# Optimization experiments

Hardware: AMD Instinct MI355X
Metric: run time of the kernel (lower is better)

The kernel has to match this reference:

```python
import jax, jax.numpy as jnp
import numpy as np

N_NODES = 20000
N_EDGES = 320000
N_GRAPHS = 64
IN_DIM = 768
HID = 256
HEADS = 4
NUM_CLASSES = 5
NEG_SLOPE = 0.2  # PyG GATConv default leaky_relu slope


def setup_inputs() -> dict:
    key = jax.random.key(0)
    ks = jax.random.split(key, 20)
    x = jax.random.normal(ks[0], (N_NODES, IN_DIM), dtype=jnp.float32)
    edge_index = jax.random.randint(ks[1], (2, N_EDGES), 0, N_NODES, dtype=jnp.int32)
    batch = jnp.sort(jax.random.randint(ks[2], (N_NODES,), 0, N_GRAPHS, dtype=jnp.int32))
    s = lambda k, sh: jax.random.normal(k, sh, dtype=jnp.float32) * (1.0 / np.sqrt(sh[0]))
    HC = HEADS * HID
    return {
        "x": x, "edge_index": edge_index, "batch": batch,
        "Wp": s(ks[3], (IN_DIM, HID)), "bp": jnp.zeros((HID,), jnp.float32),
        "W1": s(ks[4], (HID, HC)),
        "as1": jax.random.normal(ks[5], (HEADS, HID)) * 0.1,
        "ad1": jax.random.normal(ks[6], (HEADS, HID)) * 0.1,
        "b1": jnp.zeros((HC,), jnp.float32),
        "W2": s(ks[7], (HC, HC)),
        "as2": jax.random.normal(ks[8], (HEADS, HID)) * 0.1,
        "ad2": jax.random.normal(ks[9], (HEADS, HID)) * 0.1,
        "b2": jnp.zeros((HC,), jnp.float32),
        "Wc1": s(ks[10], (2 * HC, 256)), "bc1": jnp.zeros((256,), jnp.float32),
        "Wc2": s(ks[11], (256, NUM_CLASSES)), "bc2": jnp.zeros((NUM_CLASSES,), jnp.float32),
    }


def _gat(h, src, dst, W, att_s, att_d, bias):
    # PyG GATConv (concat=True), dropout in eval mode (identity).
    N = h.shape[0]
    hW = (h @ W).reshape(N, HEADS, HID)             # [N,H,C]
    a_s = jnp.einsum('nhc,hc->nh', hW, att_s)        # per-node src score
    a_d = jnp.einsum('nhc,hc->nh', hW, att_d)
    e = jax.nn.leaky_relu(a_s[src] + a_d[dst], NEG_SLOPE)  # [E,H]
    # segment softmax over incoming edges of each destination node
    m = jax.ops.segment_max(e, dst, num_segments=N)
    e = jnp.exp(e - m[dst])
    denom = jax.ops.segment_sum(e, dst, num_segments=N)
    alpha = e / (denom[dst] + 1e-16)
    msg = hW[src] * alpha[:, :, None]                # [E,H,C]
    out = jax.ops.segment_sum(msg, dst, num_segments=N)
    return out.reshape(N, HEADS * HID) + bias


def reference(x, edge_index, batch, Wp, bp, W1, as1, ad1, b1, W2, as2, ad2, b2, Wc1, bc1, Wc2, bc2):
    N = x.shape[0]
    # add self-loops (PyG GATConv default add_self_loops=True)
    loop = jnp.arange(N, dtype=edge_index.dtype)
    src = jnp.concatenate([edge_index[0], loop])
    dst = jnp.concatenate([edge_index[1], loop])

    h = jax.nn.relu(x @ Wp + bp)
    h = jax.nn.elu(_gat(h, src, dst, W1, as1, ad1, b1))
    h = jax.nn.elu(_gat(h, src, dst, W2, as2, ad2, b2))

    # global mean / max pool over graphs
    cnt = jax.ops.segment_sum(jnp.ones((N,), h.dtype), batch, num_segments=N_GRAPHS)
    mean_pool = jax.ops.segment_sum(h, batch, num_segments=N_GRAPHS) / jnp.maximum(cnt, 1.0)[:, None]
    max_pool = jax.ops.segment_max(h, batch, num_segments=N_GRAPHS)
    g = jnp.concatenate([mean_pool, max_pool], axis=1)  # [G, 2*H*C]

    hcls = jax.nn.relu(g @ Wc1 + bc1)
    return hcls @ Wc2 + bc2
```

## Files before the change

kernel.cpp:

```cpp
#include <hip/hip_runtime.h>
#include <hip/hip_fp16.h>
#include <math.h>

#define N_HID 256
#define N_HEADS 4
#define N_HC 1024
#define N_GRAPHS 64

typedef __attribute__((ext_vector_type(4))) float f32x4;
typedef _Float16 half8 __attribute__((ext_vector_type(8)));
typedef _Float16 half4 __attribute__((ext_vector_type(4)));

__device__ __forceinline__ void gl_lds16h(const __half* g, __half* l) {
    __builtin_amdgcn_global_load_lds(
        (const __attribute__((address_space(1))) unsigned int*)g,
        (__attribute__((address_space(3))) unsigned int*)l, 16, 0, 0);
}

__global__ __launch_bounds__(256) void k_deg(const int* __restrict__ dst, int E,
                                             int* __restrict__ deg) {
    int e = blockIdx.x * 256 + threadIdx.x;
    if (e < E) atomicAdd(&deg[dst[e]], 1);
}

__global__ __launch_bounds__(1024) void k_scan(const int* __restrict__ deg,
                                               int* __restrict__ rowstart, int N) {
    __shared__ int part[1024];
    const int t = threadIdx.x;
    const int chunk = (N + 1023) / 1024;
    const int c0 = t * chunk;
    int s = 0;
    for (int i = 0; i < chunk; i++) {
        int idx = c0 + i;
        if (idx < N) s += deg[idx];
    }
    part[t] = s;
    __syncthreads();
    for (int off = 1; off < 1024; off <<= 1) {
        int v = (t >= off) ? part[t - off] : 0;
        __syncthreads();
        part[t] += v;
        __syncthreads();
    }
    int run = (t == 0) ? 0 : part[t - 1];
    if (t == 0) rowstart[0] = 0;
    for (int i = 0; i < chunk; i++) {
        int idx = c0 + i;
        if (idx < N) {
            run += deg[idx];
            rowstart[idx + 1] = run;
        }
    }
}

__global__ __launch_bounds__(256) void k_fill(const int* __restrict__ src,
                                              const int* __restrict__ dst, int E,
                                              const int* __restrict__ rowstart,
                                              int* __restrict__ cursor,
                                              int* __restrict__ col) {
    int e = blockIdx.x * 256 + threadIdx.x;
    if (e < E) {
        int d = dst[e];
        int p = atomicAdd(&cursor[d], 1);
        col[rowstart[d] + p] = src[e];
    }
}

__global__ __launch_bounds__(256) void k_wtt(const float* __restrict__ W,
                                             __half* __restrict__ WT, int K, int N) {
    __shared__ float tile[32][33];
    const int k0 = blockIdx.y * 32, n0 = blockIdx.x * 32;
    const int tr = threadIdx.x >> 5, tc = threadIdx.x & 31;
#pragma unroll
    for (int rr = 0; rr < 4; rr++) {
        int k = k0 + tr + rr * 8;
        tile[tr + rr * 8][tc] = W[(size_t)k * N + n0 + tc];
    }
    __syncthreads();
#pragma unroll
    for (int rr = 0; rr < 4; rr++) {
        int n = n0 + tr + rr * 8;
        WT[(size_t)n * K + k0 + tc] = __float2half(tile[tc][tr + rr * 8]);
    }
}

__global__ __launch_bounds__(256) void k_makeva(const __half* __restrict__ W1T,
                                                const float* __restrict__ as1,
                                                const float* __restrict__ ad1,
                                                float* __restrict__ va) {
    __shared__ float satt[256];
    int b = blockIdx.x;
    int h = b & 3, isd = b >> 2;
    int k = threadIdx.x;
    const float* att = (isd ? ad1 : as1) + h * 256;
    satt[k] = att[k];
    __syncthreads();
    const __half* wr = W1T + (size_t)(h * 256) * 256 + k;
    float s = 0.f;
    for (int c = 0; c < 256; c++) s += __half2float(wr[(size_t)c * 256]) * satt[c];
    va[b * 256 + k] = s;
}

__global__ __launch_bounds__(256) void k_makeva2(const __half* __restrict__ W2T,
                                                 const float* __restrict__ as2,
                                                 const float* __restrict__ ad2,
                                                 float* __restrict__ va2) {
    __shared__ float satt[256];
    int b = blockIdx.x;
    int h = b & 3;
    int t = threadIdx.x;
    const float* att = (b >= 4 ? ad2 : as2) + h * 256;
    satt[t] = att[t];
    __syncthreads();
    float s0 = 0.f, s1 = 0.f, s2 = 0.f, s3 = 0.f;
    const __half* base = W2T + (size_t)(h * 256) * 1024 + t * 4;
    for (int j = 0; j < 256; j++) {
        half4 wv = *reinterpret_cast<const half4*>(base + (size_t)j * 1024);
        float a = satt[j];
        s0 += a * (float)wv[0]; s1 += a * (float)wv[1];
        s2 += a * (float)wv[2]; s3 += a * (float)wv[3];
    }
    *(float4*)&va2[b * 1024 + t * 4] = make_float4(s0, s1, s2, s3);
}

template <int EPI, int COSCHED>
__global__ __launch_bounds__(256) void k_gemm2p(
    const __half* __restrict__ A, const __half* __restrict__ BT,
    const float* __restrict__ bias, __half* __restrict__ C,
    int M, int NROW, int K, int lda, int ldc,
    int aoffz, int boffz, int coffz, int bofz) {
    __shared__ __half sA[2][128 * 32];
    __shared__ __half sB[2][128 * 32];
    int bm, bn;
    size_t coff = 0;
    if (COSCHED) {
        const int bid = blockIdx.x;
        const int xcd = bid & 7, j0 = bid >> 3;
        const int br = xcd + 8 * (j0 >> 3);
        const int bc = j0 & 7;
        if (br >= NROW) return;
        bm = br * 128; bn = bc * 128;
    } else {
        const int z = blockIdx.z;
        A += (size_t)z * aoffz;
        BT += (size_t)z * boffz;
        bias += z * bofz;
        coff = (size_t)z * coffz;
        bm = blockIdx.y * 128; bn = blockIdx.x * 128;
    }
    const int tid = threadIdx.x, lane = tid & 63, w = tid >> 6;
    const int wr = (w >> 1) * 64, wc = (w & 1) * 64;
    const bool isB = (w >= 2);
    const __half* gsrc = isB ? (BT + (size_t)bn * K) : (A + (size_t)bm * lda);
    const int gld = isB ? K : lda;
    const int rbase = (w & 1) * 64;
    const int lr = lane >> 2, lsl = lane & 3;
    const int g = lane >> 4, fr = lane & 15;
    const int nt = K >> 5;

    f32x4 acc[4][4] = {};

    auto STAGE = [&](int b, int t) {
        __half* sbuf = (isB ? sB[b] : sA[b]);
        const int k0 = t << 5;
#pragma unroll
        for (int c2 = 0; c2 < 4; c2++) {
            int row = rbase + c2 * 16 + lr;
            int slg = lsl ^ ((row >> 1) & 3);
            gl_lds16h(gsrc + (size_t)row * gld + k0 + slg * 8,
                      sbuf + (rbase + c2 * 16) * 32);
        }
    };

    STAGE(0, 0);
    __syncthreads();
    int cur = 0;
    for (int t = 0; t < nt; ++t) {
        if (t + 1 < nt) STAGE(cur ^ 1, t + 1);
        half8 af[4], bf[4];
#pragma unroll
        for (int i = 0; i < 4; i++) {
            int Ra = wr + i * 16 + fr;
            af[i] = *reinterpret_cast<const half8*>(
                &sA[cur][Ra * 32 + ((g ^ ((Ra >> 1) & 3)) << 3)]);
            int Rb = wc + i * 16 + fr;
            bf[i] = *reinterpret_cast<const half8*>(
                &sB[cur][Rb * 32 + ((g ^ ((Rb >> 1) & 3)) << 3)]);
        }
#pragma unroll
        for (int i = 0; i < 4; i++)
#pragma unroll
            for (int j = 0; j < 4; j++)
                acc[i][j] = __builtin_amdgcn_mfma_f32_16x16x32_f16(af[i], bf[j], acc[i][j], 0, 0, 0);
        __syncthreads();
        cur ^= 1;
    }
    const int crow0 = (lane >> 4) * 4, ccol = lane & 15;
#pragma unroll
    for (int i = 0; i < 4; i++)
#pragma unroll
        for (int j = 0; j < 4; j++) {
            int cc = bn + wc + j * 16 + ccol;
            float bv = (EPI == 2) ? bias[cc] : 0.f;
#pragma unroll
            for (int r = 0; r < 4; r++) {
                int row = bm + wr + i * 16 + crow0 + r;
                if (row < M) {
                    float v = acc[i][j][r];
                    if (EPI == 2) { v += bv; v = v > 0.f ? v : (__expf(v) - 1.f); }
                    C[(size_t)row * ldc + coff + cc] = __float2half(v);
                }
            }
        }
}

__global__ __launch_bounds__(256) void k_gemm_x(
    const float* __restrict__ A, const __half* __restrict__ BT,
    const float* __restrict__ bias, __half* __restrict__ C,
    int M, int NROW, int K, int lda) {
    __shared__ __half sA[128 * 32];
    __shared__ __half sB[128 * 32];
    const int bid = blockIdx.x;
    const int xcd = bid & 7, j0 = bid >> 3;
    const int br = xcd + 8 * (j0 >> 1);
    const int bc = j0 & 1;
    if (br >= NROW) return;
    const int bm = br * 128, bn = bc * 128;
    const int tid = threadIdx.x, lane = tid & 63, w = tid >> 6;
    const int wr = (w >> 1) * 64, wc = (w & 1) * 64;
    const int sm = tid >> 1, skb = (tid & 1) * 16;
    const bool rok = (bm + sm) < M;
    const int ph0 = (((tid & 1) * 2 + 0) ^ ((sm >> 1) & 3)) << 3;
    const int ph1 = (((tid & 1) * 2 + 1) ^ ((sm >> 1) & 3)) << 3;
    const int lr = lane >> 2, lsl = lane & 3;

    f32x4 acc[4][4] = {};

    for (int k0 = 0; k0 < K; k0 += 32) {
#pragma unroll
        for (int c = 0; c < 2; c++) {
            int rb = (w + c * 4) * 16;
            int row = rb + lr;
            int slg = lsl ^ ((row >> 1) & 3);
            gl_lds16h(BT + (size_t)(bn + row) * K + k0 + slg * 8, sB + rb * 32);
        }
        {
            const float* Arow = A + (size_t)(bm + sm) * lda + k0 + skb;
            float4 v0 = make_float4(0.f, 0.f, 0.f, 0.f), v1 = v0, v2 = v0, v3 = v0;
            if (rok) {
                v0 = *(const float4*)(Arow + 0);
                v1 = *(const float4*)(Arow + 4);
                v2 = *(const float4*)(Arow + 8);
                v3 = *(const float4*)(Arow + 12);
            }
            half8 ha, hb;
            ha[0] = (_Float16)v0.x; ha[1] = (_Float16)v0.y;
            ha[2] = (_Float16)v0.z; ha[3] = (_Float16)v0.w;
            ha[4] = (_Float16)v1.x; ha[5] = (_Float16)v1.y;
            ha[6] = (_Float16)v1.z; ha[7] = (_Float16)v1.w;
            hb[0] = (_Float16)v2.x; hb[1] = (_Float16)v2.y;
            hb[2] = (_Float16)v2.z; hb[3] = (_Float16)v2.w;
            hb[4] = (_Float16)v3.x; hb[5] = (_Float16)v3.y;
            hb[6] = (_Float16)v3.z; hb[7] = (_Float16)v3.w;
            *reinterpret_cast<half8*>(&sA[sm * 32 + ph0]) = ha;
            *reinterpret_cast<half8*>(&sA[sm * 32 + ph1]) = hb;
        }
        __syncthreads();
        half8 af[4], bf[4];
        const int g = lane >> 4, fr = lane & 15;
#pragma unroll
        for (int i = 0; i < 4; i++) {
            int Ra = wr + i * 16 + fr;
            af[i] = *reinterpret_cast<const half8*>(
                &sA[Ra * 32 + ((g ^ ((Ra >> 1) & 3)) << 3)]);
            int Rb = wc + i * 16 + fr;
            bf[i] = *reinterpret_cast<const half8*>(
                &sB[Rb * 32 + ((g ^ ((Rb >> 1) & 3)) << 3)]);
        }
#pragma unroll
        for (int i = 0; i < 4; i++)
#pragma unroll
            for (int j = 0; j < 4; j++)
                acc[i][j] = __builtin_amdgcn_mfma_f32_16x16x32_f16(af[i], bf[j], acc[i][j], 0, 0, 0);
        __syncthreads();
    }
    const int crow0 = (lane >> 4) * 4, ccol = lane & 15;
#pragma unroll
    for (int i = 0; i < 4; i++)
#pragma unroll
        for (int j = 0; j < 4; j++) {
            int cc = bn + wc + j * 16 + ccol;
            float bv = bias[cc];
#pragma unroll
            for (int r = 0; r < 4; r++) {
                int row = bm + wr + i * 16 + crow0 + r;
                if (row < M) {
                    float v = acc[i][j][r] + bv;
                    v = v > 0.f ? v : 0.f;
                    C[(size_t)row * 256 + cc] = __float2half(v);
                }
            }
        }
}

__global__ __launch_bounds__(256) void k_score8(const __half* __restrict__ h0,
                                                const float* __restrict__ va,
                                                float* __restrict__ a_s,
                                                float* __restrict__ a_d, int N) {
    __shared__ float sva[8][256];
    int t = threadIdx.x;
    for (int i = t; i < 2048; i += 256) sva[i >> 8][i & 255] = va[i];
    __syncthreads();
    int wv = t >> 6, lane = t & 63;
    int n = blockIdx.x * 4 + wv;
    if (n >= N) return;
    uint2 u = *(const uint2*)(h0 + (size_t)n * 256 + lane * 4);
    __half2 q0 = __builtin_bit_cast(__half2, u.x);
    __half2 q1 = __builtin_bit_cast(__half2, u.y);
    float v0 = __half2float(q0.x), v1 = __half2float(q0.y);
    float v2 = __half2float(q1.x), v3 = __half2float(q1.y);
    float p[8];
#pragma unroll
    for (int v = 0; v < 8; v++) {
        p[v] = v0 * sva[v][lane * 4] + v1 * sva[v][lane * 4 + 1] +
               v2 * sva[v][lane * 4 + 2] + v3 * sva[v][lane * 4 + 3];
    }
#pragma unroll
    for (int off = 32; off > 0; off >>= 1)
#pragma unroll
        for (int v = 0; v < 8; v++) p[v] += __shfl_xor(p[v], off, 64);
    if (lane == 0) {
        *(float4*)&a_s[n * 4] = make_float4(p[0], p[1], p[2], p[3]);
        *(float4*)&a_d[n * 4] = make_float4(p[4], p[5], p[6], p[7]);
    }
}

__global__ __launch_bounds__(256) void k_score1024(const __half* __restrict__ h1,
                                                   const float* __restrict__ va2,
                                                   float* __restrict__ a_s,
                                                   float* __restrict__ a_d, int N) {
    __shared__ float sva[8 * 1024];
    int t = threadIdx.x;
    for (int i = t; i < 8192; i += 256) sva[i] = va2[i];
    __syncthreads();
    int wv = t >> 6, lane = t & 63;
    int n = blockIdx.x * 4 + wv;
    if (n >= N) return;
    const __half* hp = h1 + (size_t)n * 1024;
    float hv[16];
#pragma unroll
    for (int seg = 0; seg < 4; seg++) {
        half4 u = *reinterpret_cast<const half4*>(hp + seg * 256 + lane * 4);
#pragma unroll
        for (int c = 0; c < 4; c++) hv[seg * 4 + c] = (float)u[c];
    }
    float p[8] = {};
#pragma unroll
    for (int v = 0; v < 8; v++) {
#pragma unroll
        for (int seg = 0; seg < 4; seg++) {
            float4 f = *(const float4*)&sva[v * 1024 + seg * 256 + lane * 4];
            p[v] += hv[seg * 4] * f.x + hv[seg * 4 + 1] * f.y +
                    hv[seg * 4 + 2] * f.z + hv[seg * 4 + 3] * f.w;
        }
    }
#pragma unroll
    for (int off = 32; off > 0; off >>= 1)
#pragma unroll
        for (int v = 0; v < 8; v++) p[v] += __shfl_xor(p[v], off, 64);
    if (lane == 0) {
        *(float4*)&a_s[n * 4] = make_float4(p[0], p[1], p[2], p[3]);
        *(float4*)&a_d[n * 4] = make_float4(p[4], p[5], p[6], p[7]);
    }
}

__global__ __launch_bounds__(256) void k_gat_w1(
    const __half* __restrict__ h0, const float* __restrict__ a_s,
    const float* __restrict__ a_d, const int* __restrict__ rowstart,
    const int* __restrict__ col, __half* __restrict__ agg1, int N) {
    __shared__ int wsn[4][64];
    __shared__ float wal[4][64][2];
    const int w = threadIdx.x >> 6, lane = threadIdx.x & 63;
    const int ni = w >> 1, q = w & 1;
    const int n = blockIdx.x * 2 + ni;
    if (n >= N) return;
    const int hh0 = q * 2;
    const int e0 = rowstart[n];
    const int deg = rowstart[n + 1] - e0;
    const int tot = deg + 1;
    const float adv0 = a_d[n * 4 + hh0], adv1 = a_d[n * 4 + hh0 + 1];
    float M0 = -INFINITY, M1 = -INFINITY, S0 = 0.f, S1 = 0.f;
    float acc0[4] = {}, acc1[4] = {};

    for (int base = 0; base < tot; base += 64) {
        const int cnt = min(64, tot - base);
        const bool act = lane < cnt;
        int sn = n;
        float ev0 = -INFINITY, ev1 = -INFINITY;
        if (act) {
            const int li = base + lane;
            sn = (li < deg) ? col[e0 + li] : n;
            float s0 = a_s[sn * 4 + hh0] + adv0;
            float s1 = a_s[sn * 4 + hh0 + 1] + adv1;
            ev0 = s0 >= 0.f ? s0 : 0.2f * s0;
            ev1 = s1 >= 0.f ? s1 : 0.2f * s1;
        }
        float m0 = ev0, m1 = ev1;
#pragma unroll
        for (int off = 32; off > 0; off >>= 1) {
            m0 = fmaxf(m0, __shfl_xor(m0, off, 64));
            m1 = fmaxf(m1, __shfl_xor(m1, off, 64));
        }
        m0 = fmaxf(m0, M0); m1 = fmaxf(m1, M1);
        float w0 = act ? __expf(ev0 - m0) : 0.f;
        float w1 = act ? __expf(ev1 - m1) : 0.f;
        wsn[w][lane] = sn;
        wal[w][lane][0] = w0;
        wal[w][lane][1] = w1;
        float s0 = w0, s1 = w1;
#pragma unroll
        for (int off = 32; off > 0; off >>= 1) {
            s0 += __shfl_xor(s0, off, 64);
            s1 += __shfl_xor(s1, off, 64);
        }
        float sc0 = __expf(M0 - m0), sc1 = __expf(M1 - m1);
        S0 = S0 * sc0 + s0; S1 = S1 * sc1 + s1;
        M0 = m0; M1 = m1;
#pragma unroll
        for (int c = 0; c < 4; c++) { acc0[c] *= sc0; acc1[c] *= sc1; }
#pragma unroll 2
        for (int i = 0; i < cnt; i++) {
            const int s2 = wsn[w][i];
            const float a0 = wal[w][i][0], a1 = wal[w][i][1];
            uint2 u = *(const uint2*)(h0 + (size_t)s2 * 256 + lane * 4);
            __half2 p0 = __builtin_bit_cast(__half2, u.x);
            __half2 p1 = __builtin_bit_cast(__half2, u.y);
            const float v[4] = {__half2float(p0.x), __half2float(p0.y),
                                __half2float(p1.x), __half2float(p1.y)};
#pragma unroll
            for (int c = 0; c < 4; c++) {
                acc0[c] += a0 * v[c];
                acc1[c] += a1 * v[c];
            }
        }
    }
    const float d0 = 1.f / (S0 + 1e-16f), d1 = 1.f / (S1 + 1e-16f);
    half4 o0, o1;
#pragma unroll
    for (int c = 0; c < 4; c++) {
        o0[c] = (_Float16)(acc0[c] * d0);
        o1[c] = (_Float16)(acc1[c] * d1);
    }
    *reinterpret_cast<half4*>(agg1 + (size_t)n * 1024 + hh0 * 256 + lane * 4) = o0;
    *reinterpret_cast<half4*>(agg1 + (size_t)n * 1024 + (hh0 + 1) * 256 + lane * 4) = o1;
}

__global__ __launch_bounds__(256) void k_gat_w2(
    const __half* __restrict__ hW, const float* __restrict__ a_s,
    const float* __restrict__ a_d, const int* __restrict__ rowstart,
    const int* __restrict__ col, const float* __restrict__ bias,
    __half* __restrict__ h2, int N) {
    __shared__ int wsn[4][64];
    __shared__ float wal[4][64][2];
    const int w = threadIdx.x >> 6, lane = threadIdx.x & 63;
    const int ni = w >> 1, q = w & 1;
    const int n = blockIdx.x * 2 + ni;
    if (n >= N) return;
    const int hh0 = q * 2;
    const int hiq = lane >> 5;
    const int e0 = rowstart[n];
    const int deg = rowstart[n + 1] - e0;
    const int tot = deg + 1;
    const float adv0 = a_d[n * 4 + hh0], adv1 = a_d[n * 4 + hh0 + 1];
    float M0 = -INFINITY, M1 = -INFINITY, S0 = 0.f, S1 = 0.f;
    float acc[8] = {};

    for (int base = 0; base < tot; base += 64) {
        const int cnt = min(64, tot - base);
        const bool act = lane < cnt;
        int sn = n;
        float ev0 = -INFINITY, ev1 = -INFINITY;
        if (act) {
            const int li = base + lane;
            sn = (li < deg) ? col[e0 + li] : n;
            float s0 = a_s[sn * 4 + hh0] + adv0;
            float s1 = a_s[sn * 4 + hh0 + 1] + adv1;
            ev0 = s0 >= 0.f ? s0 : 0.2f * s0;
            ev1 = s1 >= 0.f ? s1 : 0.2f * s1;
        }
        float m0 = ev0, m1 = ev1;
#pragma unroll
        for (int off = 32; off > 0; off >>= 1) {
            m0 = fmaxf(m0, __shfl_xor(m0, off, 64));
            m1 = fmaxf(m1, __shfl_xor(m1, off, 64));
        }
        m0 = fmaxf(m0, M0); m1 = fmaxf(m1, M1);
        float w0 = act ? __expf(ev0 - m0) : 0.f;
        float w1 = act ? __expf(ev1 - m1) : 0.f;
        wsn[w][lane] = sn;
        wal[w][lane][0] = w0;
        wal[w][lane][1] = w1;
        float s0 = w0, s1 = w1;
#pragma unroll
        for (int off = 32; off > 0; off >>= 1) {
            s0 += __shfl_xor(s0, off, 64);
            s1 += __shfl_xor(s1, off, 64);
        }
        float sc0 = __expf(M0 - m0), sc1 = __expf(M1 - m1);
        S0 = S0 * sc0 + s0; S1 = S1 * sc1 + s1;
        M0 = m0; M1 = m1;
        const float accsc = hiq ? sc1 : sc0;
#pragma unroll
        for (int c = 0; c < 8; c++) acc[c] *= accsc;
        const __half* gbase = hW + q * 512 + lane * 8;
#pragma unroll 2
        for (int i = 0; i < cnt; i++) {
            const int s2 = wsn[w][i];
            const float a = wal[w][i][hiq];
            half8 v = *reinterpret_cast<const half8*>(gbase + (size_t)s2 * 1024);
#pragma unroll
            for (int c = 0; c < 8; c++) acc[c] += a * (float)v[c];
        }
    }
    const float S = hiq ? S1 : S0;
    const float d = 1.f / (S + 1e-16f);
    const int chb = q * 512 + lane * 8;
    float4 b0 = *(const float4*)&bias[chb];
    float4 b1 = *(const float4*)&bias[chb + 4];
    const float bb[8] = {b0.x, b0.y, b0.z, b0.w, b1.x, b1.y, b1.z, b1.w};
    half8 o;
#pragma unroll
    for (int c = 0; c < 8; c++) {
        float v = acc[c] * d + bb[c];
        v = v > 0.f ? v : (__expf(v) - 1.f);
        o[c] = (_Float16)v;
    }
    *reinterpret_cast<half8*>(h2 + (size_t)n * 1024 + chb) = o;
}

__global__ __launch_bounds__(128) void k_gbounds(const int* __restrict__ batch, int N,
                                                 int* __restrict__ gstart) {
    int g = threadIdx.x;
    if (g > N_GRAPHS) return;
    if (g == N_GRAPHS) { gstart[N_GRAPHS] = N; return; }
    int lo = 0, hi = N;
    while (lo < hi) {
        int mid = (lo + hi) >> 1;
        if (batch[mid] < g) lo = mid + 1; else hi = mid;
    }
    gstart[g] = lo;
}

__global__ __launch_bounds__(128) void k_pool(const __half* __restrict__ h,
                                              const int* __restrict__ gstart,
                                              float* __restrict__ gout) {
    int g = blockIdx.x, t = threadIdx.x;
    int c = blockIdx.y * 256 + 2 * t;
    int s = gstart[g], e = gstart[g + 1];
    float s0 = 0.f, s1 = 0.f;
    float m0 = -INFINITY, m1 = -INFINITY;
    for (int i = s; i < e; i++) {
        __half2 hv = *(const __half2*)(h + (size_t)i * N_HC + c);
        float v0 = __half2float(hv.x), v1 = __half2float(hv.y);
        s0 += v0; s1 += v1;
        m0 = fmaxf(m0, v0); m1 = fmaxf(m1, v1);
    }
    float cnt = fmaxf((float)(e - s), 1.f);
    *(float2*)(gout + (size_t)g * 2048 + c) = make_float2(s0 / cnt, s1 / cnt);
    *(float2*)(gout + (size_t)g * 2048 + 1024 + c) = make_float2(m0, m1);
}

__global__ __launch_bounds__(256) void k_cls1(const float* __restrict__ g,
                                              const float* __restrict__ Wc1,
                                              const float* __restrict__ bc1,
                                              float* __restrict__ hcls) {
    __shared__ float gs[2048];
    int gb = blockIdx.x, t = threadIdx.x;
    for (int i = t; i < 2048; i += 256) gs[i] = g[(size_t)gb * 2048 + i];
    __syncthreads();
    float acc = 0.f;
    for (int k = 0; k < 2048; k++) acc += gs[k] * Wc1[(size_t)k * 256 + t];
    float v = acc + bc1[t];
    hcls[gb * 256 + t] = v > 0.f ? v : 0.f;
}

__global__ __launch_bounds__(256) void k_cls2(const float* __restrict__ hcls,
                                              const float* __restrict__ Wc2,
                                              const float* __restrict__ bc2,
                                              float* __restrict__ out) {
    int idx = blockIdx.x * 256 + threadIdx.x;
    if (idx >= N_GRAPHS * 5) return;
    int gb = idx / 5, j = idx % 5;
    float acc = 0.f;
    for (int k = 0; k < 256; k++) acc += hcls[gb * 256 + k] * Wc2[k * 5 + j];
    out[idx] = acc + bc2[j];
}

extern "C" void kernel_launch(void* const* d_in, const int* in_sizes, int n_in,
                              void* d_out, int out_size, void* d_ws, size_t ws_size,
                              hipStream_t stream) {
    const float* x    = (const float*)d_in[0];
    const int*   ei   = (const int*)d_in[1];
    const int*   batch= (const int*)d_in[2];
    const float* Wp   = (const float*)d_in[3];
    const float* bp   = (const float*)d_in[4];
    const float* W1   = (const float*)d_in[5];
    const float* as1  = (const float*)d_in[6];
    const float* ad1  = (const float*)d_in[7];
    const float* b1   = (const float*)d_in[8];
    const float* W2   = (const float*)d_in[9];
    const float* as2  = (const float*)d_in[10];
    const float* ad2  = (const float*)d_in[11];
    const float* b2   = (const float*)d_in[12];
    const float* Wc1  = (const float*)d_in[13];
    const float* bc1  = (const float*)d_in[14];
    const float* Wc2  = (const float*)d_in[15];
    const float* bc2  = (const float*)d_in[16];
    float* out = (float*)d_out;

    const int N = in_sizes[0] / 768;
    const int E = in_sizes[1] / 2;
    const int MP = ((N + 127) / 128) * 128;
    const int MB = MP / 128;

    const int* src = ei;
    const int* dst = ei + E;

    char* ws = (char*)d_ws;
    size_t off = 0;
    auto give = [&](size_t bytes) -> void* {
        void* p = ws + off;
        off = (off + bytes + 255) & ~(size_t)255;
        return p;
    };
    __half* h0  = (__half*)give((size_t)MP * N_HID * 2);
    __half* agg1= (__half*)give((size_t)MP * N_HC * 2);
    __half* h1  = (__half*)give((size_t)MP * N_HC * 2);
    __half* hW2 = (__half*)give((size_t)MP * N_HC * 2);
    __half* h2  = (__half*)give((size_t)MP * N_HC * 2);
    __half* WpT = (__half*)give((size_t)768 * 256 * 2);
    __half* W1T = (__half*)give((size_t)256 * 1024 * 2);
    __half* W2T = (__half*)give((size_t)1024 * 1024 * 2);
    float* va   = (float*)give((size_t)8 * 256 * 4);
    float* va2  = (float*)give((size_t)8 * 1024 * 4);
    float* a_s1 = (float*)give((size_t)N * N_HEADS * 4);
    float* a_d1 = (float*)give((size_t)N * N_HEADS * 4);
    float* a_s2 = (float*)give((size_t)N * N_HEADS * 4);
    float* a_d2 = (float*)give((size_t)N * N_HEADS * 4);
    int* deg     = (int*)give((size_t)N * 4);
    int* cursor  = (int*)give((size_t)N * 4);
    int* rowstart= (int*)give((size_t)(N + 1) * 4);
    int* col     = (int*)give((size_t)E * 4);
    int* gstart  = (int*)give((size_t)(N_GRAPHS + 1) * 4);
    float* gpool = (float*)give((size_t)N_GRAPHS * 2048 * 4);
    float* hcls  = (float*)give((size_t)N_GRAPHS * 256 * 4);
    (void)ws_size; (void)n_in; (void)out_size;

    hipMemsetAsync(deg, 0, (size_t)N * 4, stream);
    hipMemsetAsync(cursor, 0, (size_t)N * 4, stream);
    k_deg<<<(E + 255) / 256, 256, 0, stream>>>(dst, E, deg);
    k_scan<<<1, 1024, 0, stream>>>(deg, rowstart, N);
    k_fill<<<(E + 255) / 256, 256, 0, stream>>>(src, dst, E, rowstart, cursor, col);
    k_gbounds<<<1, 128, 0, stream>>>(batch, N, gstart);

    k_wtt<<<dim3(256 / 32, 768 / 32), 256, 0, stream>>>(Wp, WpT, 768, 256);
    k_wtt<<<dim3(1024 / 32, 256 / 32), 256, 0, stream>>>(W1, W1T, 256, 1024);
    k_wtt<<<dim3(1024 / 32, 1024 / 32), 256, 0, stream>>>(W2, W2T, 1024, 1024);
    k_makeva<<<8, 256, 0, stream>>>(W1T, as1, ad1, va);
    k_makeva2<<<8, 256, 0, stream>>>(W2T, as2, ad2, va2);

    const int NROWPAD = ((MB + 7) / 8) * 8;

    k_gemm_x<<<NROWPAD * 2, 256, 0, stream>>>(x, WpT, bp, h0, N, MB, 768, 768);

    k_score8<<<(N + 3) / 4, 256, 0, stream>>>(h0, va, a_s1, a_d1, N);
    k_gat_w1<<<(N + 1) / 2, 256, 0, stream>>>(h0, a_s1, a_d1, rowstart, col, agg1, N);
    k_gemm2p<2, 0><<<dim3(2, MB, 4), 256, 0, stream>>>(
        agg1, W1T, b1, h1, N, 0, 256, 1024, 1024, 256, 65536, 256, 256);

    k_score1024<<<(N + 3) / 4, 256, 0, stream>>>(h1, va2, a_s2, a_d2, N);
    k_gemm2p<0, 1><<<NROWPAD * 8, 256, 0, stream>>>(
        h1, W2T, nullptr, hW2, N, MB, 1024, 1024, 1024, 0, 0, 0, 0);
    k_gat_w2<<<(N + 1) / 2, 256, 0, stream>>>(hW2, a_s2, a_d2, rowstart, col, b2, h2, N);

    k_pool<<<dim3(N_GRAPHS, 4), 128, 0, stream>>>(h2, gstart, gpool);
    k_cls1<<<N_GRAPHS, 256, 0, stream>>>(gpool, Wc1, bc1, hcls);
    k_cls2<<<2, 256, 0, stream>>>(hcls, Wc2, bc2, out);
}
```

Baseline: 557.0 us.

## Use partial vmcnt waits in GEMM loop and remap layer-2 aggregation to per-head blocks

The GEMM main loop drops __syncthreads and instead issues an explicit s_waitcnt vmcnt(4) plus s_barrier. This lets the prefetch of the next K tile stay in flight while the current tile is consumed, removing the full drain of outstanding loads each iteration. Separately, the layer-2 GAT aggregation kernel now assigns one wave per node per head, using half4 loads and one softmax stream, instead of two heads per wave with half8 loads. That gives more blocks and simpler per-wave softmax, but each wave makes narrower gathers and the per-edge score and index work is repeated per head. The hand-written vmcnt count depends on how many global_load_lds each thread issues in STAGE (4 here), so it is fragile if that count changes.

```diff
diff --git a/kernel.cpp b/kernel.cpp
--- a/kernel.cpp
+++ b/kernel.cpp
@@ -173,10 +173,15 @@
     };
 
     STAGE(0, 0);
-    __syncthreads();
     int cur = 0;
     for (int t = 0; t < nt; ++t) {
-        if (t + 1 < nt) STAGE(cur ^ 1, t + 1);
+        if (t + 1 < nt) {
+            STAGE(cur ^ 1, t + 1);
+            asm volatile("s_waitcnt vmcnt(4)" ::: "memory");
+        } else {
+            asm volatile("s_waitcnt vmcnt(0)" ::: "memory");
+        }
+        asm volatile("s_barrier" ::: "memory");
         half8 af[4], bf[4];
 #pragma unroll
         for (int i = 0; i < 4; i++) {
@@ -192,7 +197,7 @@
 #pragma unroll
             for (int j = 0; j < 4; j++)
                 acc[i][j] = __builtin_amdgcn_mfma_f32_16x16x32_f16(af[i], bf[j], acc[i][j], 0, 0, 0);
-        __syncthreads();
+        asm volatile("s_barrier" ::: "memory");
         cur ^= 1;
     }
     const int crow0 = (lane >> 4) * 4, ccol = lane & 15;
@@ -461,81 +466,69 @@
     const int* __restrict__ col, const float* __restrict__ bias,
     __half* __restrict__ h2, int N) {
     __shared__ int wsn[4][64];
-    __shared__ float wal[4][64][2];
+    __shared__ float wal[4][64];
     const int w = threadIdx.x >> 6, lane = threadIdx.x & 63;
-    const int ni = w >> 1, q = w & 1;
-    const int n = blockIdx.x * 2 + ni;
+    const int bid = blockIdx.x;
+    const int h = bid & 3;
+    const int n = (bid >> 2) * 4 + w;
     if (n >= N) return;
-    const int hh0 = q * 2;
-    const int hiq = lane >> 5;
     const int e0 = rowstart[n];
     const int deg = rowstart[n + 1] - e0;
     const int tot = deg + 1;
-    const float adv0 = a_d[n * 4 + hh0], adv1 = a_d[n * 4 + hh0 + 1];
-    float M0 = -INFINITY, M1 = -INFINITY, S0 = 0.f, S1 = 0.f;
-    float acc[8] = {};
+    const float adv = a_d[n * 4 + h];
+    float M = -INFINITY, S = 0.f;
+    float acc[4] = {};
 
     for (int base = 0; base < tot; base += 64) {
         const int cnt = min(64, tot - base);
         const bool act = lane < cnt;
         int sn = n;
-        float ev0 = -INFINITY, ev1 = -INFINITY;
+        float ev = -INFINITY;
         if (act) {
             const int li = base + lane;
             sn = (li < deg) ? col[e0 + li] : n;
-            float s0 = a_s[sn * 4 + hh0] + adv0;
-            float s1 = a_s[sn * 4 + hh0 + 1] + adv1;
-            ev0 = s0 >= 0.f ? s0 : 0.2f * s0;
-            ev1 = s1 >= 0.f ? s1 : 0.2f * s1;
-        }
-        float m0 = ev0, m1 = ev1;
-#pragma unroll
-        for (int off = 32; off > 0; off >>= 1) {
-            m0 = fmaxf(m0, __shfl_xor(m0, off, 64));
-            m1 = fmaxf(m1, __shfl_xor(m1, off, 64));
-        }
-        m0 = fmaxf(m0, M0); m1 = fmaxf(m1, M1);
-        float w0 = act ? __expf(ev0 - m0) : 0.f;
-        float w1 = act ? __expf(ev1 - m1) : 0.f;
+            float s = a_s[sn * 4 + h] + adv;
+            ev = s >= 0.f ? s : 0.2f * s;
+        }
+        float m = ev;
+#pragma unroll
+        for (int off = 32; off > 0; off >>= 1)
+            m = fmaxf(m, __shfl_xor(m, off, 64));
+        m = fmaxf(m, M);
+        float wv = act ? __expf(ev - m) : 0.f;
         wsn[w][lane] = sn;
-        wal[w][lane][0] = w0;
-        wal[w][lane][1] = w1;
-        float s0 = w0, s1 = w1;
-#pragma unroll
-        for (int off = 32; off > 0; off >>= 1) {
-            s0 += __shfl_xor(s0, off, 64);
-            s1 += __shfl_xor(s1, off, 64);
-        }
-        float sc0 = __expf(M0 - m0), sc1 = __expf(M1 - m1);
-        S0 = S0 * sc0 + s0; S1 = S1 * sc1 + s1;
-        M0 = m0; M1 = m1;
-        const float accsc = hiq ? sc1 : sc0;
-#pragma unroll
-        for (int c = 0; c < 8; c++) acc[c] *= accsc;
-        const __half* gbase = hW + q * 512 + lane * 8;
+        wal[w][lane] = wv;
+        float sw = wv;
+#pragma unroll
+        for (int off = 32; off > 0; off >>= 1)
+            sw += __shfl_xor(sw, off, 64);
+        float sc = __expf(M - m);
+        S = S * sc + sw;
+        M = m;
+#pragma unroll
+        for (int c = 0; c < 4; c++) acc[c] *= sc;
+        const __half* gbase = hW + h * 256 + lane * 4;
 #pragma unroll 2
         for (int i = 0; i < cnt; i++) {
             const int s2 = wsn[w][i];
-            const float a = wal[w][i][hiq];
-            half8 v = *reinterpret_cast<const half8*>(gbase + (size_t)s2 * 1024);
-#pragma unroll
-            for (int c = 0; c < 8; c++) acc[c] += a * (float)v[c];
-        }
-    }
-    const float S = hiq ? S1 : S0;
+            const float a = wal[w][i];
+            half4 v = *reinterpret_cast<const half4*>(gbase + (size_t)s2 * 1024);
+#pragma unroll
+            for (int c = 0; c < 4; c++) acc[c] += a * (float)v[c];
+        }
+    }
     const float d = 1.f / (S + 1e-16f);
-    const int chb = q * 512 + lane * 8;
-    float4 b0 = *(const float4*)&bias[chb];
-    float4 b1 = *(const float4*)&bias[chb + 4];
-    const float bb[8] = {b0.x, b0.y, b0.z, b0.w, b1.x, b1.y, b1.z, b1.w};
-    half8 o;
-#pragma unroll
-    for (int c = 0; c < 8; c++) {
-        float v = acc[c] * d + bb[c];
+    const int cc = h * 256 + lane * 4;
+    float4 bb = *(const float4*)&bias[cc];
+    const float bv[4] = {bb.x, bb.y, bb.z, bb.w};
+    half4 o;
+#pragma unroll
+    for (int c = 0; c < 4; c++) {
+        float v = acc[c] * d + bv[c];
         v = v > 0.f ? v : (__expf(v) - 1.f);
         o[c] = (_Float16)v;
     }
-    *reinterpret_cast<half8*>(h2 + (size_t)n * 1024 + chb) = o;
+    *reinterpret_cast<half4*>(h2 + (size_t)n * 1024 + cc) = o;
 }
 
 __global__ __launch_bounds__(128) void k_gbounds(const int* __restrict__ batch, int N,
@@ -681,7 +674,8 @@
     k_score1024<<<(N + 3) / 4, 256, 0, stream>>>(h1, va2, a_s2, a_d2, N);
     k_gemm2p<0, 1><<<NROWPAD * 8, 256, 0, stream>>>(
         h1, W2T, nullptr, hW2, N, MB, 1024, 1024, 1024, 0, 0, 0, 0);
-    k_gat_w2<<<(N + 1) / 2, 256, 0, stream>>>(hW2, a_s2, a_d2, rowstart, col, b2, h2, N);
+    k_gat_w2<<<((N + 3) / 4) * 4, 256, 0, stream>>>(
+        hW2, a_s2, a_d2, rowstart, col, b2, h2, N);
 
     k_pool<<<dim3(N_GRAPHS, 4), 128, 0, stream>>>(h2, gstart, gpool);
     k_cls1<<<N_GRAPHS, 256, 0, stream>>>(gpool, Wc1, bc1, hcls);
```

Result: faster. 536.8 us (-3.6%).
